# Optimization experiments

Measured on AMD Instinct MI355X. Metric: run time of the kernel, lower is better.

The kernel has to match this reference:

```python
import jax, jax.numpy as jnp
import numpy as np
from jax import lax

V, E, H, T, S = 100000, 256, 512, 9, 4096
HH = H // 2
START, STOP = 7, 8
NEG = -10000.0


def setup_inputs() -> dict:
    key = jax.random.key(0)
    ks = jax.random.split(key, 16)
    def n(k, shape, scale=0.1):
        return jax.random.normal(k, shape, jnp.float32) * scale
    sentence = jax.random.randint(ks[0], (S,), 0, V)
    embed = n(ks[1], (V, E), 1.0)
    w_ih_f = n(ks[2], (4 * HH, E)); w_hh_f = n(ks[3], (4 * HH, HH))
    b_ih_f = n(ks[4], (4 * HH,));   b_hh_f = n(ks[5], (4 * HH,))
    w_ih_b = n(ks[6], (4 * HH, E)); w_hh_b = n(ks[7], (4 * HH, HH))
    b_ih_b = n(ks[8], (4 * HH,));   b_hh_b = n(ks[9], (4 * HH,))
    h0 = n(ks[10], (2, HH), 1.0)  # init_hidden: randn (2,1,HH), batch squeezed
    c0 = n(ks[11], (2, HH), 1.0)
    W_out = n(ks[12], (T, H)); b_out = n(ks[13], (T,))
    transitions = jax.random.normal(ks[14], (T, T), jnp.float32)
    transitions = transitions.at[START, :].set(NEG).at[:, STOP].set(NEG)
    return dict(sentence=sentence, embed=embed,
                w_ih_f=w_ih_f, w_hh_f=w_hh_f, b_ih_f=b_ih_f, b_hh_f=b_hh_f,
                w_ih_b=w_ih_b, w_hh_b=w_hh_b, b_ih_b=b_ih_b, b_hh_b=b_hh_b,
                h0=h0, c0=c0, W_out=W_out, b_out=b_out, transitions=transitions)


def _lstm_dir(x_gates, h0, c0, w_hh):
    # x_gates: [S, 4*HH] = x @ w_ih.T + b_ih + b_hh (precomputed input part)
    def step(carry, xg):
        h, c = carry
        g = xg + h @ w_hh.T
        i, f, gg, o = jnp.split(g, 4)  # torch gate order: i, f, g, o
        i = jax.nn.sigmoid(i); f = jax.nn.sigmoid(f)
        gg = jnp.tanh(gg);     o = jax.nn.sigmoid(o)
        c = f * c + i * gg
        h = o * jnp.tanh(c)
        return (h, c), h
    _, hs = lax.scan(step, (h0, c0), x_gates)
    return hs  # [S, HH]


def reference(sentence, embed, w_ih_f, w_hh_f, b_ih_f, b_hh_f,
              w_ih_b, w_hh_b, b_ih_b, b_hh_b, h0, c0, W_out, b_out, transitions):
    x = embed[sentence]  # [S, E]
    # bidirectional LSTM, batch=1
    hf = _lstm_dir(x @ w_ih_f.T + b_ih_f + b_hh_f, h0[0], c0[0], w_hh_f)
    hb = _lstm_dir((x @ w_ih_b.T + b_ih_b + b_hh_b)[::-1], h0[1], c0[1], w_hh_b)[::-1]
    lstm_out = jnp.concatenate([hf, hb], axis=-1)          # [S, H]
    frames = lstm_out @ W_out.T + b_out                     # [S, T] emission scores

    # Viterbi-style decode (faithful: alpha updated by logsumexp, backpointers by argmax)
    alpha0 = jnp.full((T,), NEG, jnp.float32).at[START].set(0.0)
    def vstep(alpha, frame):
        smat = alpha[:, None] + frame[None, :] + transitions  # [T, T]
        bp = jnp.argmax(smat, axis=0)
        return jax.nn.logsumexp(smat, axis=0), bp
    alpha, bps = lax.scan(vstep, alpha0, frames)            # bps: [S, T]

    final = alpha + transitions[:, STOP]                     # [T]
    best = jnp.argmax(final)
    score = jax.nn.logsumexp(final)

    # backtrack over bps[1:] in reverse
    def bstep(tag, bp):
        nt = bp[tag]
        return nt, nt
    _, path_rev = lax.scan(bstep, best, bps[1:][::-1])
    tag_seq = jnp.concatenate([path_rev[::-1], best[None]])  # [S]
    return score, tag_seq
```

## Files before the change

### kernel.cpp

```cpp
#include <hip/hip_runtime.h>
#include <hip/hip_bf16.h>

#define SEQ   4096
#define EMB   256
#define HHID  256
#define G4    1024
#define NT    9
#define TSTART 7
#define TSTOP  8
#define NEGV  (-10000.0f)
#define POISON 0xAAAAAAAAu

#define WS_XG_F   0u
#define WS_XG_B   16777216u
#define WS_HF     33554432u
#define WS_HB     37748736u
#define WS_FRAMES 41943040u

#define PIDX(c) ((((c) >> 5) * 36) + ((c) & 31))

__global__ __launch_bounds__(256) void xgate_kernel(
    const int* __restrict__ sentence, const float* __restrict__ embed,
    const float* __restrict__ w_ih_f, const float* __restrict__ b_ih_f,
    const float* __restrict__ b_hh_f,
    const float* __restrict__ w_ih_b, const float* __restrict__ b_ih_b,
    const float* __restrict__ b_hh_b,
    float* __restrict__ xg_f, float* __restrict__ xg_b)
{
    const int st  = blockIdx.x;
    const int dir = blockIdx.y;
    const float* w  = dir ? w_ih_b : w_ih_f;
    const float* bi = dir ? b_ih_b : b_ih_f;
    const float* bh = dir ? b_hh_b : b_hh_f;
    float* xg = dir ? xg_b : xg_f;
    const int t = threadIdx.x;

    __shared__ float x_t[EMB][16];
    for (int sl = 0; sl < 16; ++sl) {
        int s   = st * 16 + sl;
        int tok = sentence[s];
        x_t[t][sl] = embed[(size_t)tok * EMB + t];
    }
    __syncthreads();

    float acc[4][16];
    #pragma unroll
    for (int q = 0; q < 4; ++q)
        #pragma unroll
        for (int sl = 0; sl < 16; ++sl) acc[q][sl] = 0.f;

    #pragma unroll 4
    for (int e = 0; e < EMB; ++e) {
        float w0 = w[(size_t)(t        ) * EMB + e];
        float w1 = w[(size_t)(t + 256  ) * EMB + e];
        float w2 = w[(size_t)(t + 512  ) * EMB + e];
        float w3 = w[(size_t)(t + 768  ) * EMB + e];
        #pragma unroll
        for (int sl = 0; sl < 16; ++sl) {
            float xv = x_t[e][sl];
            acc[0][sl] += w0 * xv;
            acc[1][sl] += w1 * xv;
            acc[2][sl] += w2 * xv;
            acc[3][sl] += w3 * xv;
        }
    }

    #pragma unroll
    for (int q = 0; q < 4; ++q) {
        int g = t + 256 * q;
        float bb = bi[g] + bh[g];
        for (int sl = 0; sl < 16; ++sl) {
            xg[(size_t)(st * 16 + sl) * G4 + g] = acc[q][sl] + bb;
        }
    }
}

__global__ __launch_bounds__(256, 1) void lstm_kernel(
    const float* __restrict__ xg_f, const float* __restrict__ xg_b,
    const float* __restrict__ w_hh_f, const float* __restrict__ w_hh_b,
    const float* __restrict__ h0, const float* __restrict__ c0,
    float* __restrict__ hf, float* __restrict__ hb)
{
    const int bx    = blockIdx.x;
    const int dir   = bx >> 3;
    const int slice = bx & 7;
    const int t     = threadIdx.x;
    const int cb    = t & 7;
    const int rb    = t >> 3;
    const int unit  = slice * 32 + rb;

    const float* xg   = dir ? xg_b  : xg_f;
    const float* w_hh = dir ? w_hh_b : w_hh_f;
    float* hout = dir ? hb : hf;

    __shared__ float buf[2][288];

    float wa[128];
    #pragma unroll
    for (int q = 0; q < 4; ++q) {
        #pragma unroll
        for (int j = 0; j < 32; ++j) {
            float tmp = w_hh[(size_t)(q * HHID + unit) * HHID + cb * 32 + j];
            asm volatile("v_accvgpr_write_b32 %0, %1"
                         : "=a"(wa[q * 32 + j]) : "v"(tmp));
        }
    }

    float c_reg = 0.f;
    if (cb == 0) c_reg = c0[dir * HHID + unit];

    const bool own = (t >= slice * 32) && (t < slice * 32 + 32);

    for (int n = 0; n < SEQ; ++n) {
        const int s = dir ? (SEQ - 1 - n) : n;

        float xg0 = 0.f, xg1 = 0.f, xg2 = 0.f, xg3 = 0.f;
        if (cb == 0) {
            const float* xb = xg + (size_t)s * G4 + unit;
            xg0 = xb[0];
            xg1 = xb[HHID];
            xg2 = xb[2 * HHID];
            xg3 = xb[3 * HHID];
        }

        if (n == 0) {
            buf[0][PIDX(t)] = h0[dir * HHID + t];
        } else if (!own) {
            const int sp = dir ? (s + 1) : (s - 1);
            const unsigned int* src =
                (const unsigned int*)(hout + (size_t)sp * HHID) + t;
            unsigned v = __hip_atomic_load(src, __ATOMIC_RELAXED,
                                           __HIP_MEMORY_SCOPE_AGENT);
            while (v == POISON) {
                __builtin_amdgcn_s_sleep(1);
                v = __hip_atomic_load(src, __ATOMIC_RELAXED,
                                      __HIP_MEMORY_SCOPE_AGENT);
            }
            buf[n & 1][PIDX(t)] = __uint_as_float(v);
        }
        __syncthreads();

        float a0 = 0.f, a1 = 0.f, a2 = 0.f, a3 = 0.f;
        const float4* h4 = (const float4*)(&buf[n & 1][cb * 36]);
        #pragma unroll
        for (int j4 = 0; j4 < 8; ++j4) {
            float4 hv = h4[j4];
            #pragma unroll
            for (int k = 0; k < 4; ++k) {
                float hk = (k == 0) ? hv.x : (k == 1) ? hv.y
                         : (k == 2) ? hv.z : hv.w;
                float w0, w1, w2, w3;
                asm volatile("v_accvgpr_read_b32 %0, %1"
                             : "=v"(w0) : "a"(wa[0 * 32 + j4 * 4 + k]));
                asm volatile("v_accvgpr_read_b32 %0, %1"
                             : "=v"(w1) : "a"(wa[1 * 32 + j4 * 4 + k]));
                asm volatile("v_accvgpr_read_b32 %0, %1"
                             : "=v"(w2) : "a"(wa[2 * 32 + j4 * 4 + k]));
                asm volatile("v_accvgpr_read_b32 %0, %1"
                             : "=v"(w3) : "a"(wa[3 * 32 + j4 * 4 + k]));
                a0 += w0 * hk;
                a1 += w1 * hk;
                a2 += w2 * hk;
                a3 += w3 * hk;
            }
        }

        #pragma unroll
        for (int m = 1; m <= 4; m <<= 1) {
            a0 += __shfl_xor(a0, m);
            a1 += __shfl_xor(a1, m);
            a2 += __shfl_xor(a2, m);
            a3 += __shfl_xor(a3, m);
        }

        if (cb == 0) {
            float gi = a0 + xg0;
            float gf = a1 + xg1;
            float gg = a2 + xg2;
            float go = a3 + xg3;
            float iv = 1.f / (1.f + __expf(-gi));
            float fv = 1.f / (1.f + __expf(-gf));
            float gv = 1.f - 2.f / (__expf(2.f * gg) + 1.f);
            float ov = 1.f / (1.f + __expf(-go));
            float c  = fv * c_reg + iv * gv;
            c_reg = c;
            float h  = ov * (1.f - 2.f / (__expf(2.f * c) + 1.f));
            unsigned int* dst =
                (unsigned int*)(hout + (size_t)s * HHID) + unit;
            __hip_atomic_store(dst, __float_as_uint(h), __ATOMIC_RELAXED,
                               __HIP_MEMORY_SCOPE_AGENT);
            buf[(n + 1) & 1][PIDX(unit)] = h;
        }
    }
}

__global__ __launch_bounds__(256) void frames_kernel(
    const float* __restrict__ hf, const float* __restrict__ hb,
    const float* __restrict__ W_out, const float* __restrict__ b_out,
    float* __restrict__ frames)
{
    int o = blockIdx.x * 256 + threadIdx.x;
    if (o >= SEQ * NT) return;
    int s = o / NT;
    int j = o - s * NT;
    const float4* a0 = (const float4*)(hf + (size_t)s * HHID);
    const float4* a1 = (const float4*)(hb + (size_t)s * HHID);
    const float4* w0 = (const float4*)(W_out + (size_t)j * 512);
    const float4* w1 = w0 + 64;
    float acc = 0.f;
    #pragma unroll 8
    for (int i = 0; i < 64; ++i) {
        float4 a = a0[i], b = w0[i];
        acc += a.x * b.x + a.y * b.y + a.z * b.z + a.w * b.w;
        float4 c = a1[i], d = w1[i];
        acc += c.x * d.x + c.y * d.y + c.z * d.z + c.w * d.w;
    }
    frames[o] = acc + b_out[j];
}

__global__ __launch_bounds__(64) void crf_kernel(
    const float* __restrict__ frames, const float* __restrict__ trans,
    float* __restrict__ dout)
{
    __shared__ float fr[512 * NT];
    __shared__ unsigned char bpl[SEQ * NT];
    const int t = threadIdx.x;
    const int tc = (t < NT) ? t : 0;

    float trow[NT];
    #pragma unroll
    for (int i = 0; i < NT; ++i) trow[i] = 0.f;
    if (t < NT) {
        #pragma unroll
        for (int i = 0; i < NT; ++i) trow[i] = trans[i * NT + t];
    }
    float alpha = (t == TSTART) ? 0.f : NEGV;

    for (int chunk = 0; chunk < 8; ++chunk) {
        for (int idx = t; idx < 512 * NT; idx += 64)
            fr[idx] = frames[chunk * 512 * NT + idx];
        __syncthreads();

        for (int sl = 0; sl < 512; ++sl) {
            const int s = chunk * 512 + sl;
            float v[NT];
            #pragma unroll
            for (int i = 0; i < NT; ++i)
                v[i] = __shfl(alpha, i) + trow[i];
            float mx = v[0];
            int   am = 0;
            #pragma unroll
            for (int i = 1; i < NT; ++i)
                if (v[i] > mx) { mx = v[i]; am = i; }
            float sum = 0.f;
            #pragma unroll
            for (int i = 0; i < NT; ++i) sum += __expf(v[i] - mx);
            float anew = fr[sl * NT + tc] + mx + __logf(sum);
            if (t < NT) {
                bpl[s * NT + t] = (unsigned char)am;
                alpha = anew;
            }
        }
        __syncthreads();
    }

    float fin = NEGV;
    if (t < NT) fin = alpha + trans[t * NT + TSTOP];
    float f[NT];
    #pragma unroll
    for (int j = 0; j < NT; ++j) f[j] = __shfl(fin, j);

    if (t == 0) {
        float mx = f[0];
        int best = 0;
        #pragma unroll
        for (int j = 1; j < NT; ++j)
            if (f[j] > mx) { mx = f[j]; best = j; }
        float sum = 0.f;
        #pragma unroll
        for (int j = 0; j < NT; ++j) sum += __expf(f[j] - mx);
        dout[0] = mx + __logf(sum);

        int cur = best;
        dout[1 + SEQ - 1] = (float)cur;
        for (int s = SEQ - 2; s >= 0; --s) {
            cur = bpl[(s + 1) * NT + cur];
            dout[1 + s] = (float)cur;
        }
    }
}

extern "C" void kernel_launch(void* const* d_in, const int* in_sizes, int n_in,
                              void* d_out, int out_size, void* d_ws, size_t ws_size,
                              hipStream_t stream)
{
    const int*   sentence = (const int*)  d_in[0];
    const float* embed    = (const float*)d_in[1];
    const float* w_ih_f   = (const float*)d_in[2];
    const float* w_hh_f   = (const float*)d_in[3];
    const float* b_ih_f   = (const float*)d_in[4];
    const float* b_hh_f   = (const float*)d_in[5];
    const float* w_ih_b   = (const float*)d_in[6];
    const float* w_hh_b   = (const float*)d_in[7];
    const float* b_ih_b   = (const float*)d_in[8];
    const float* b_hh_b   = (const float*)d_in[9];
    const float* h0       = (const float*)d_in[10];
    const float* c0       = (const float*)d_in[11];
    const float* W_out    = (const float*)d_in[12];
    const float* b_out    = (const float*)d_in[13];
    const float* trans    = (const float*)d_in[14];

    float* out = (float*)d_out;
    char*  ws  = (char*)d_ws;

    float* xg_f   = (float*)(ws + WS_XG_F);
    float* xg_b   = (float*)(ws + WS_XG_B);
    float* hf     = (float*)(ws + WS_HF);
    float* hb     = (float*)(ws + WS_HB);
    float* frames = (float*)(ws + WS_FRAMES);

    hipMemsetAsync(hf, 0xAA, 2u * SEQ * HHID * sizeof(float), stream);

    xgate_kernel<<<dim3(256, 2), 256, 0, stream>>>(
        sentence, embed, w_ih_f, b_ih_f, b_hh_f, w_ih_b, b_ih_b, b_hh_b,
        xg_f, xg_b);

    lstm_kernel<<<16, 256, 0, stream>>>(
        xg_f, xg_b, w_hh_f, w_hh_b, h0, c0, hf, hb);

    frames_kernel<<<(SEQ * NT + 255) / 256, 256, 0, stream>>>(
        hf, hb, W_out, b_out, frames);

    crf_kernel<<<1, 64, 0, stream>>>(frames, trans, out);
}
```

Measured before the change: 10.01 ms.

## Interleave gate pre-activations per unit and pipeline spin-wait polling loads

The input-gate kernel now loads weights as float4 and writes the four gate values of each hidden unit contiguously, so the recurrent kernel can fetch all four gates with a single float4 load per step. The spin-wait on the previous step's hidden state now keeps several atomic loads in flight instead of sleeping between single polls, which should cut latency on the serial critical path. The cost is more memory traffic while polling and a changed intermediate layout that both kernels must agree on.

```diff
diff --git a/kernel.cpp b/kernel.cpp
--- a/kernel.cpp
+++ b/kernel.cpp
@@ -49,29 +49,39 @@
         #pragma unroll
         for (int sl = 0; sl < 16; ++sl) acc[q][sl] = 0.f;
 
-    #pragma unroll 4
-    for (int e = 0; e < EMB; ++e) {
-        float w0 = w[(size_t)(t        ) * EMB + e];
-        float w1 = w[(size_t)(t + 256  ) * EMB + e];
-        float w2 = w[(size_t)(t + 512  ) * EMB + e];
-        float w3 = w[(size_t)(t + 768  ) * EMB + e];
-        #pragma unroll
-        for (int sl = 0; sl < 16; ++sl) {
-            float xv = x_t[e][sl];
-            acc[0][sl] += w0 * xv;
-            acc[1][sl] += w1 * xv;
-            acc[2][sl] += w2 * xv;
-            acc[3][sl] += w3 * xv;
-        }
-    }
-
-    #pragma unroll
-    for (int q = 0; q < 4; ++q) {
-        int g = t + 256 * q;
-        float bb = bi[g] + bh[g];
-        for (int sl = 0; sl < 16; ++sl) {
-            xg[(size_t)(st * 16 + sl) * G4 + g] = acc[q][sl] + bb;
-        }
+    const float4* wr0 = (const float4*)(w + (size_t)(t      ) * EMB);
+    const float4* wr1 = (const float4*)(w + (size_t)(t + 256) * EMB);
+    const float4* wr2 = (const float4*)(w + (size_t)(t + 512) * EMB);
+    const float4* wr3 = (const float4*)(w + (size_t)(t + 768) * EMB);
+    #pragma unroll 2
+    for (int e4 = 0; e4 < EMB / 4; ++e4) {
+        float4 w0 = wr0[e4], w1 = wr1[e4], w2 = wr2[e4], w3 = wr3[e4];
+        #pragma unroll
+        for (int k = 0; k < 4; ++k) {
+            float f0 = (k == 0) ? w0.x : (k == 1) ? w0.y : (k == 2) ? w0.z : w0.w;
+            float f1 = (k == 0) ? w1.x : (k == 1) ? w1.y : (k == 2) ? w1.z : w1.w;
+            float f2 = (k == 0) ? w2.x : (k == 1) ? w2.y : (k == 2) ? w2.z : w2.w;
+            float f3 = (k == 0) ? w3.x : (k == 1) ? w3.y : (k == 2) ? w3.z : w3.w;
+            int e = e4 * 4 + k;
+            #pragma unroll
+            for (int sl = 0; sl < 16; ++sl) {
+                float xv = x_t[e][sl];
+                acc[0][sl] += f0 * xv;
+                acc[1][sl] += f1 * xv;
+                acc[2][sl] += f2 * xv;
+                acc[3][sl] += f3 * xv;
+            }
+        }
+    }
+
+    float bb0 = bi[t      ] + bh[t      ];
+    float bb1 = bi[t + 256] + bh[t + 256];
+    float bb2 = bi[t + 512] + bh[t + 512];
+    float bb3 = bi[t + 768] + bh[t + 768];
+    for (int sl = 0; sl < 16; ++sl) {
+        float4 val = make_float4(acc[0][sl] + bb0, acc[1][sl] + bb1,
+                                 acc[2][sl] + bb2, acc[3][sl] + bb3);
+        ((float4*)(xg + (size_t)(st * 16 + sl) * G4))[t] = val;
     }
 }
 
@@ -114,13 +124,9 @@
     for (int n = 0; n < SEQ; ++n) {
         const int s = dir ? (SEQ - 1 - n) : n;
 
-        float xg0 = 0.f, xg1 = 0.f, xg2 = 0.f, xg3 = 0.f;
+        float4 xgv = make_float4(0.f, 0.f, 0.f, 0.f);
         if (cb == 0) {
-            const float* xb = xg + (size_t)s * G4 + unit;
-            xg0 = xb[0];
-            xg1 = xb[HHID];
-            xg2 = xb[2 * HHID];
-            xg3 = xb[3 * HHID];
+            xgv = *(const float4*)(xg + (size_t)s * G4 + 4u * unit);
         }
 
         if (n == 0) {
@@ -131,10 +137,33 @@
                 (const unsigned int*)(hout + (size_t)sp * HHID) + t;
             unsigned v = __hip_atomic_load(src, __ATOMIC_RELAXED,
                                            __HIP_MEMORY_SCOPE_AGENT);
-            while (v == POISON) {
-                __builtin_amdgcn_s_sleep(1);
-                v = __hip_atomic_load(src, __ATOMIC_RELAXED,
-                                      __HIP_MEMORY_SCOPE_AGENT);
+            if (v == POISON) {
+                unsigned q0, q1, q2, q3;
+                q0 = __hip_atomic_load(src, __ATOMIC_RELAXED,
+                                       __HIP_MEMORY_SCOPE_AGENT);
+                __builtin_amdgcn_s_sleep(2);
+                q1 = __hip_atomic_load(src, __ATOMIC_RELAXED,
+                                       __HIP_MEMORY_SCOPE_AGENT);
+                __builtin_amdgcn_s_sleep(2);
+                q2 = __hip_atomic_load(src, __ATOMIC_RELAXED,
+                                       __HIP_MEMORY_SCOPE_AGENT);
+                __builtin_amdgcn_s_sleep(2);
+                q3 = __hip_atomic_load(src, __ATOMIC_RELAXED,
+                                       __HIP_MEMORY_SCOPE_AGENT);
+                for (;;) {
+                    if (q0 != POISON) { v = q0; break; }
+                    q0 = __hip_atomic_load(src, __ATOMIC_RELAXED,
+                                           __HIP_MEMORY_SCOPE_AGENT);
+                    if (q1 != POISON) { v = q1; break; }
+                    q1 = __hip_atomic_load(src, __ATOMIC_RELAXED,
+                                           __HIP_MEMORY_SCOPE_AGENT);
+                    if (q2 != POISON) { v = q2; break; }
+                    q2 = __hip_atomic_load(src, __ATOMIC_RELAXED,
+                                           __HIP_MEMORY_SCOPE_AGENT);
+                    if (q3 != POISON) { v = q3; break; }
+                    q3 = __hip_atomic_load(src, __ATOMIC_RELAXED,
+                                           __HIP_MEMORY_SCOPE_AGENT);
+                }
             }
             buf[n & 1][PIDX(t)] = __uint_as_float(v);
         }
@@ -174,10 +203,10 @@
         }
 
         if (cb == 0) {
-            float gi = a0 + xg0;
-            float gf = a1 + xg1;
-            float gg = a2 + xg2;
-            float go = a3 + xg3;
+            float gi = a0 + xgv.x;
+            float gf = a1 + xgv.y;
+            float gg = a2 + xgv.z;
+            float go = a3 + xgv.w;
             float iv = 1.f / (1.f + __expf(-gi));
             float fv = 1.f / (1.f + __expf(-gf));
             float gv = 1.f - 2.f / (__expf(2.f * gg) + 1.f);
```

Result: no change. 9.914 ms (-1.0%).
